# Optimization experiments

Measured on AMD Instinct MI355X. Metric: run time of the kernel, lower is better.

The kernel has to match this reference:

```python
import jax, jax.numpy as jnp
import numpy as np

PI = float(np.pi)


def setup_inputs() -> dict:
    key = jax.random.key(0)
    k1, k2 = jax.random.split(key)
    src = jax.random.normal(k1, (32, 4, 512, 512), dtype=jnp.float32)
    fc2 = jax.random.normal(k2, (32, 7), dtype=jnp.float32)
    return {"src": src, "fc2": fc2}


def _build_mat(fc2):
    # Parameter extraction exactly as in the torch module.
    theta = jnp.clip(fc2[:, 0] * 0.3, -1.0, 1.0) * PI          # rotation angle
    scale = jnp.clip(fc2[:, 1:3] * 0.3 + 1.0, 0.0, 5.0)
    trans = fc2[:, 3:5] * 0.3
    shear = jnp.clip(fc2[:, 5:7] * 0.3, -1.0, 1.0) * PI
    sx, sy = scale[:, 0], scale[:, 1]
    tx, ty = trans[:, 0], trans[:, 1]
    shxy, shyx = shear[:, 0], shear[:, 1]
    c, s = jnp.cos(theta), jnp.sin(theta)
    z, o = jnp.zeros_like(c), jnp.ones_like(c)

    def m3(rows):  # rows: list of 3 lists of 3 (B,) scalars -> (B,3,3)
        return jnp.stack([jnp.stack(r, axis=-1) for r in rows], axis=-2)

    # Note: the torch code stacks rows at dim=2 (making the transpose) then
    # transposes (1,2) back, so the effective matrices are the ones as-written.
    rot = m3([[c, -s, z], [s, c, z], [z, z, o]])
    scl = m3([[sx, z, z], [z, sy, z], [z, z, o]])
    shr = m3([[o, shxy, z], [shyx, o, z], [z, z, o]])
    trn = m3([[o, z, tx], [z, o, ty], [z, z, o]])
    # mat = T @ Sh @ S @ R  (batched 3x3 matmuls)
    return trn @ shr @ scl @ rot


def _affine_grid(theta2x3, H, W):
    # F.affine_grid with align_corners=False (the torch default used here):
    # pixel centers map to x=(2w+1)/W-1, y=(2h+1)/H-1.
    xs = (2.0 * jnp.arange(W, dtype=jnp.float32) + 1.0) / W - 1.0  # (W,)
    ys = (2.0 * jnp.arange(H, dtype=jnp.float32) + 1.0) / H - 1.0  # (H,)
    base = jnp.stack([
        jnp.broadcast_to(xs[None, :], (H, W)),
        jnp.broadcast_to(ys[:, None], (H, W)),
        jnp.ones((H, W), dtype=jnp.float32),
    ], axis=-1)                                                     # (H,W,3)
    return jnp.einsum('bij,hwj->bhwi', theta2x3, base)              # (B,H,W,2)


def _grid_sample(src, grid):
    # bilinear, padding_mode='zeros', align_corners=False
    B, C, H, W = src.shape
    ix = ((grid[..., 0] + 1.0) * W - 1.0) * 0.5  # (B,H,W) source x coords
    iy = ((grid[..., 1] + 1.0) * H - 1.0) * 0.5
    x0 = jnp.floor(ix)
    y0 = jnp.floor(iy)
    wx = ix - x0  # frac weights
    wy = iy - y0
    x0i = x0.astype(jnp.int32)
    y0i = y0.astype(jnp.int32)

    def gather(img, xi, yi):  # img (C,H,W); xi,yi (H,W) int
        valid = ((xi >= 0) & (xi < W) & (yi >= 0) & (yi < H)).astype(img.dtype)
        v = img[:, jnp.clip(yi, 0, H - 1), jnp.clip(xi, 0, W - 1)]  # (C,H,W)
        return v * valid[None]

    def per_batch(img, x0i, y0i, wx, wy):
        v00 = gather(img, x0i, y0i)
        v01 = gather(img, x0i + 1, y0i)
        v10 = gather(img, x0i, y0i + 1)
        v11 = gather(img, x0i + 1, y0i + 1)
        return (v00 * (1 - wx) * (1 - wy) + v01 * wx * (1 - wy)
                + v10 * (1 - wx) * wy + v11 * wx * wy)

    return jax.vmap(per_batch)(src, x0i, y0i, wx, wy)


def reference(src, fc2):
    H, W = src.shape[2], src.shape[3]
    mat = _build_mat(fc2)                     # (B,3,3)
    inv_mat = jnp.linalg.inv(mat)             # (B,3,3)
    grid = _affine_grid(mat[:, :2, :], H, W)
    inv_grid = _affine_grid(inv_mat[:, :2, :], H, W)
    transformed = _grid_sample(src, grid)
    return transformed, mat, inv_mat, grid, inv_grid
```

## Files before the change

### kernel.cpp

```cpp
#include <hip/hip_runtime.h>
#include <hip/hip_bf16.h>

#define PI_F 3.14159265358979323846f

__global__ void build_mats_kernel(const float* __restrict__ fc2,
                                  float* __restrict__ mat_out,
                                  float* __restrict__ inv_out,
                                  int B) {
    int b = blockIdx.x * blockDim.x + threadIdx.x;
    if (b >= B) return;
    const float* f = fc2 + b * 7;
    float theta = fminf(fmaxf(f[0] * 0.3f, -1.f), 1.f) * PI_F;
    float sx    = fminf(fmaxf(f[1] * 0.3f + 1.f, 0.f), 5.f);
    float sy    = fminf(fmaxf(f[2] * 0.3f + 1.f, 0.f), 5.f);
    float tx    = f[3] * 0.3f;
    float ty    = f[4] * 0.3f;
    float shxy  = fminf(fmaxf(f[5] * 0.3f, -1.f), 1.f) * PI_F;
    float shyx  = fminf(fmaxf(f[6] * 0.3f, -1.f), 1.f) * PI_F;

    float c = cosf(theta), s = sinf(theta);
    float m00 =  sx * c + shxy * sy * s;
    float m01 = -sx * s + shxy * sy * c;
    float m02 = tx;
    float m10 = shyx * sx * c + sy * s;
    float m11 = -shyx * sx * s + sy * c;
    float m12 = ty;

    float* m = mat_out + b * 9;
    m[0] = m00; m[1] = m01; m[2] = m02;
    m[3] = m10; m[4] = m11; m[5] = m12;
    m[6] = 0.f; m[7] = 0.f; m[8] = 1.f;

    float det = m00 * m11 - m01 * m10;
    float id  = 1.f / det;
    float i00 =  m11 * id, i01 = -m01 * id;
    float i10 = -m10 * id, i11 =  m00 * id;
    float i02 = -(i00 * m02 + i01 * m12);
    float i12 = -(i10 * m02 + i11 * m12);

    float* im = inv_out + b * 9;
    im[0] = i00; im[1] = i01; im[2] = i02;
    im[3] = i10; im[4] = i11; im[5] = i12;
    im[6] = 0.f; im[7] = 0.f; im[8] = 1.f;
}

__global__ __launch_bounds__(256) void affine_main_kernel(
    const float* __restrict__ src,
    const float* __restrict__ mat,
    const float* __restrict__ inv_mat,
    float* __restrict__ transformed,
    float* __restrict__ grid_out,
    float* __restrict__ inv_grid_out)
{
    const int W = 512, H = 512, C = 4;
    int w = blockIdx.x * blockDim.x + threadIdx.x;
    int h = blockIdx.y;
    int b = blockIdx.z;

    float xs = (2.f * (float)w + 1.f) * (1.f / (float)W) - 1.f;
    float ys = (2.f * (float)h + 1.f) * (1.f / (float)H) - 1.f;

    const float* m  = mat + b * 9;
    const float* im = inv_mat + b * 9;
    float gx  = m[0] * xs + m[1] * ys + m[2];
    float gy  = m[3] * xs + m[4] * ys + m[5];
    float igx = im[0] * xs + im[1] * ys + im[2];
    float igy = im[3] * xs + im[4] * ys + im[5];

    size_t pix = ((size_t)b * H + h) * W + w;
    ((float2*)grid_out)[pix]     = make_float2(gx, gy);
    ((float2*)inv_grid_out)[pix] = make_float2(igx, igy);

    float ix = ((gx + 1.f) * (float)W - 1.f) * 0.5f;
    float iy = ((gy + 1.f) * (float)H - 1.f) * 0.5f;
    float x0f = floorf(ix), y0f = floorf(iy);
    float wx = ix - x0f, wy = iy - y0f;
    int x0 = (int)x0f, y0 = (int)y0f;
    int x1 = x0 + 1,   y1 = y0 + 1;

    bool vx0 = (x0 >= 0) && (x0 < W);
    bool vx1 = (x1 >= 0) && (x1 < W);
    bool vy0 = (y0 >= 0) && (y0 < H);
    bool vy1 = (y1 >= 0) && (y1 < H);
    int cx0 = min(max(x0, 0), W - 1), cx1 = min(max(x1, 0), W - 1);
    int cy0 = min(max(y0, 0), H - 1), cy1 = min(max(y1, 0), H - 1);

    float w00 = (1.f - wx) * (1.f - wy) * ((vx0 && vy0) ? 1.f : 0.f);
    float w01 = wx * (1.f - wy)         * ((vx1 && vy0) ? 1.f : 0.f);
    float w10 = (1.f - wx) * wy         * ((vx0 && vy1) ? 1.f : 0.f);
    float w11 = wx * wy                 * ((vx1 && vy1) ? 1.f : 0.f);

    const float* sb = src + (size_t)b * C * H * W;
    size_t o00 = (size_t)cy0 * W + cx0;
    size_t o01 = (size_t)cy0 * W + cx1;
    size_t o10 = (size_t)cy1 * W + cx0;
    size_t o11 = (size_t)cy1 * W + cx1;

    #pragma unroll
    for (int c = 0; c < C; ++c) {
        const float* sc = sb + (size_t)c * H * W;
        float v = sc[o00] * w00 + sc[o01] * w01 + sc[o10] * w10 + sc[o11] * w11;
        transformed[(((size_t)b * C + c) * H + h) * W + w] = v;
    }
}

extern "C" void kernel_launch(void* const* d_in, const int* in_sizes, int n_in,
                              void* d_out, int out_size, void* d_ws, size_t ws_size,
                              hipStream_t stream) {
    const float* src = (const float*)d_in[0];
    const float* fc2 = (const float*)d_in[1];

    const int B = 32, C = 4, H = 512, W = 512;
    float* out = (float*)d_out;

    float* transformed  = out;
    float* mat_out      = out + (size_t)B * C * H * W;
    float* inv_out      = mat_out + (size_t)B * 9;
    float* grid_out     = inv_out + (size_t)B * 9;
    float* inv_grid_out = grid_out + (size_t)B * H * W * 2;

    build_mats_kernel<<<1, 64, 0, stream>>>(fc2, mat_out, inv_out, B);

    dim3 grid(W / 256, H, B);
    dim3 block(256);
    affine_main_kernel<<<grid, block, 0, stream>>>(src, mat_out, inv_out,
                                                   transformed, grid_out, inv_grid_out);
}
```

Before: 478.5 us.

## Use 2D 16x16 pixel tiles with nontemporal grid stores and 32-bit offsets

Each block now covers a 16x16 pixel tile built from four 8x8 sub-tiles instead of a 256-wide row strip. Because the affine map can rotate the sampling pattern, a 2D footprint should give better cache locality for the gathered source reads. The grid and inverse-grid outputs are written with nontemporal stores so they do not evict source data, and the gather offsets use 32-bit integer math. The trade-off is that output writes are now only 8 floats contiguous per row within a wavefront, which may make them less well coalesced.

```diff
diff --git a/kernel.cpp b/kernel.cpp
--- a/kernel.cpp
+++ b/kernel.cpp
@@ -2,6 +2,8 @@
 #include <hip/hip_bf16.h>
 
 #define PI_F 3.14159265358979323846f
+
+typedef float f32x2 __attribute__((ext_vector_type(2)));
 
 __global__ void build_mats_kernel(const float* __restrict__ fc2,
                                   float* __restrict__ mat_out,
@@ -53,9 +55,12 @@
     float* __restrict__ inv_grid_out)
 {
     const int W = 512, H = 512, C = 4;
-    int w = blockIdx.x * blockDim.x + threadIdx.x;
-    int h = blockIdx.y;
-    int b = blockIdx.z;
+    const int tx = threadIdx.x;
+    const int ty = threadIdx.y;
+    const int tz = threadIdx.z;
+    const int w = blockIdx.x * 16 + (tz & 1) * 8 + tx;
+    const int h = blockIdx.y * 16 + (tz >> 1) * 8 + ty;
+    const int b = blockIdx.z;
 
     float xs = (2.f * (float)w + 1.f) * (1.f / (float)W) - 1.f;
     float ys = (2.f * (float)h + 1.f) * (1.f / (float)H) - 1.f;
@@ -68,8 +73,10 @@
     float igy = im[3] * xs + im[4] * ys + im[5];
 
     size_t pix = ((size_t)b * H + h) * W + w;
-    ((float2*)grid_out)[pix]     = make_float2(gx, gy);
-    ((float2*)inv_grid_out)[pix] = make_float2(igx, igy);
+    f32x2 g2  = {gx, gy};
+    f32x2 ig2 = {igx, igy};
+    __builtin_nontemporal_store(g2,  (f32x2*)grid_out + pix);
+    __builtin_nontemporal_store(ig2, (f32x2*)inv_grid_out + pix);
 
     float ix = ((gx + 1.f) * (float)W - 1.f) * 0.5f;
     float iy = ((gy + 1.f) * (float)H - 1.f) * 0.5f;
@@ -91,14 +98,14 @@
     float w11 = wx * wy                 * ((vx1 && vy1) ? 1.f : 0.f);
 
     const float* sb = src + (size_t)b * C * H * W;
-    size_t o00 = (size_t)cy0 * W + cx0;
-    size_t o01 = (size_t)cy0 * W + cx1;
-    size_t o10 = (size_t)cy1 * W + cx0;
-    size_t o11 = (size_t)cy1 * W + cx1;
+    int o00 = cy0 * W + cx0;
+    int o01 = cy0 * W + cx1;
+    int o10 = cy1 * W + cx0;
+    int o11 = cy1 * W + cx1;
 
     #pragma unroll
     for (int c = 0; c < C; ++c) {
-        const float* sc = sb + (size_t)c * H * W;
+        const float* sc = sb + c * (H * W);
         float v = sc[o00] * w00 + sc[o01] * w01 + sc[o10] * w10 + sc[o11] * w11;
         transformed[(((size_t)b * C + c) * H + h) * W + w] = v;
     }
@@ -121,8 +128,8 @@
 
     build_mats_kernel<<<1, 64, 0, stream>>>(fc2, mat_out, inv_out, B);
 
-    dim3 grid(W / 256, H, B);
-    dim3 block(256);
+    dim3 grid(W / 16, H / 16, B);
+    dim3 block(8, 8, 4);
     affine_main_kernel<<<grid, block, 0, stream>>>(src, mat_out, inv_out,
                                                    transformed, grid_out, inv_grid_out);
 }
```

Result: faster. 460.6 us (-3.8%).
